# Kernel optimization log

Hardware: AMD Instinct MI355X
Metric: run time of the kernel (lower is better)

## Reference

```python
import jax, jax.numpy as jnp
import numpy as np

LATENT, HIDDEN, NF, MAXN = 256, 512, 64, 50
B = 128
# ordered node pairs (i, j), i != j, in the original double-loop (row-major) order
_pairs = np.array([(i, j) for i in range(MAXN) for j in range(MAXN) if i != j], dtype=np.int32)
II = jnp.asarray(_pairs[:, 0])  # [P]
JJ = jnp.asarray(_pairs[:, 1])  # [P]


def _lin_init(key, out_d, in_d):
    kw, kb = jax.random.split(key)
    s = 1.0 / np.sqrt(in_d)
    W = jax.random.uniform(kw, (out_d, in_d), jnp.float32, -s, s)
    b = jax.random.uniform(kb, (out_d,), jnp.float32, -s, s)
    return W, b


def setup_inputs() -> dict:
    key = jax.random.key(0)
    ks = jax.random.split(key, 7)
    z = jax.random.normal(ks[0], (B, LATENT), jnp.float32)
    # node decoder: latent -> hidden -> hidden -> maxn*nf
    W1, b1 = _lin_init(ks[1], HIDDEN, LATENT)
    W2, b2 = _lin_init(ks[2], HIDDEN, HIDDEN)
    W3, b3 = _lin_init(ks[3], MAXN * NF, HIDDEN)
    # edge decoder: latent + 2*nf -> hidden -> hidden//2 -> 1
    E1, c1 = _lin_init(ks[4], HIDDEN, LATENT + 2 * NF)
    E2, c2 = _lin_init(ks[5], HIDDEN // 2, HIDDEN)
    E3, c3 = _lin_init(ks[6], 1, HIDDEN // 2)
    return {"z": z, "W1": W1, "b1": b1, "W2": W2, "b2": b2, "W3": W3, "b3": b3,
            "E1": E1, "c1": c1, "E2": E2, "c2": c2, "E3": E3, "c3": c3}


def reference(z, W1, b1, W2, b2, W3, b3, E1, c1, E2, c2, E3, c3):
    # ---- node decoder ----
    h = jax.nn.relu(z @ W1.T + b1)
    h = jax.nn.relu(h @ W2.T + b2)
    node_feat = (h @ W3.T + b3).reshape(B, MAXN, NF)  # raw logits used for edges
    node_probs = jax.nn.sigmoid(node_feat)
    # ---- edge decoder: batched over all P = MAXN*(MAXN-1) ordered pairs ----
    ni = node_feat[:, II, :]  # [B, P, NF]
    nj = node_feat[:, JJ, :]  # [B, P, NF]
    P = II.shape[0]
    zb = jnp.broadcast_to(z[:, None, :], (B, P, LATENT))
    edge_in = jnp.concatenate([zb, ni, nj], axis=-1)  # [B, P, LATENT+2*NF]
    e = jax.nn.relu(jnp.einsum("bpf,hf->bph", edge_in, E1) + c1)
    e = jax.nn.relu(jnp.einsum("bph,gh->bpg", e, E2) + c2)
    edge_probs = jax.nn.sigmoid(jnp.einsum("bpg,og->bpo", e, E3) + c3)[..., 0]  # [B, P]
    return node_probs, edge_probs
```

## Files before the change

### kernel.cpp

```cpp
#include <hip/hip_runtime.h>
#include <hip/hip_bf16.h>
#include <math.h>

#define LATENT 256
#define HIDDEN 512
#define NFD    64
#define MAXN   50
#define BATCH  128
#define NPAIR  2450
#define PTILE  64
#define NTILES 39

typedef __attribute__((ext_vector_type(8))) _Float16 f16x8;
typedef __attribute__((ext_vector_type(4))) float f32x4;
typedef __attribute__((ext_vector_type(4))) unsigned int u32x4;

__device__ __forceinline__ float sigmoidf_(float x) {
    return 1.0f / (1.0f + expf(-x));
}
__device__ __forceinline__ f16x8 build_e1(f16x8 ui, f16x8 uj) {
    f16x8 s = ui + uj;
    return __builtin_elementwise_max(s, (f16x8)(_Float16)0);
}
__device__ __forceinline__ void gll16(const void* g, void* l) {
    __builtin_amdgcn_global_load_lds(
        (const __attribute__((address_space(1))) void*)g,
        (__attribute__((address_space(3))) void*)l, 16, 0, 0);
}
__device__ __forceinline__ u32x4 pack8(float4 a, float4 b) {
    f16x8 h;
    h[0] = (_Float16)a.x; h[1] = (_Float16)a.y;
    h[2] = (_Float16)a.z; h[3] = (_Float16)a.w;
    h[4] = (_Float16)b.x; h[5] = (_Float16)b.y;
    h[6] = (_Float16)b.z; h[7] = (_Float16)b.w;
    return __builtin_bit_cast(u32x4, h);
}

__global__ __launch_bounds__(256) void prologue_a(
    const float* __restrict__ z,
    const float* __restrict__ W1, const float* __restrict__ b1,
    const float* __restrict__ E1, const float* __restrict__ c1,
    const float* __restrict__ E2, const float* __restrict__ W2,
    const float* __restrict__ W3,
    unsigned short* __restrict__ E2t,
    unsigned short* __restrict__ W2h,
    unsigned short* __restrict__ W3h,
    unsigned short* __restrict__ E1ih,
    unsigned short* __restrict__ E1jh,
    unsigned short* __restrict__ h1h, float* __restrict__ Abc)
{
    const int tid = threadIdx.x;

    if (blockIdx.x >= 32) {
        int slot = (blockIdx.x - 32) * 4 + blockIdx.y;
        int e = (slot * 256 + tid) * 8;
        const float* src;
        unsigned short* dst;
        if (e < 262144) { src = W2 + e; dst = W2h + e; }
        else if (e < 1900544) { int l = e - 262144; src = W3 + l; dst = W3h + l; }
        else if (e < 1933312) {
            int l = e - 1900544; int row = l >> 6, col = l & 63;
            src = E1 + row * 384 + 256 + col; dst = E1ih + l;
        } else {
            int l = e - 1933312; int row = l >> 6, col = l & 63;
            src = E1 + row * 384 + 320 + col; dst = E1jh + l;
        }
        float4 a = *(const float4*)src;
        float4 b = *(const float4*)(src + 4);
        *(u32x4*)dst = pack8(a, b);
        return;
    }

    if (blockIdx.x >= 16) {
        int idx = ((blockIdx.x - 16) * 4 + blockIdx.y) * 256 + tid;
        int g  = idx & 255;
        int kc = idx >> 8;
        float4 a = *(const float4*)&E2[(size_t)g * 512 + kc * 8];
        float4 b = *(const float4*)&E2[(size_t)g * 512 + kc * 8 + 4];
        *(u32x4*)(E2t + (size_t)idx * 8) = pack8(a, b);
        return;
    }

    __shared__ __align__(16) float As[16][34];
    __shared__ __align__(16) float Bs[16][68];

    const int m0 = blockIdx.y * 32;
    const int n0 = blockIdx.x * 64;
    const bool isE = n0 >= 512;
    const float* Bp = isE ? E1 + (size_t)(n0 - 512) * 384 : W1 + (size_t)n0 * 256;
    const int ldb = isE ? 384 : 256;

    const int sra = tid >> 3;
    const int kca = (tid & 7) * 2;
    const int srb = tid >> 2;
    const int kcb = (tid & 3) * 4;
    const int tx = tid & 15;
    const int ty = tid >> 4;

    float acc[2][4] = {};

    for (int k0 = 0; k0 < 256; k0 += 16) {
        float2 a2 = *(const float2*)&z[(size_t)(m0 + sra) * 256 + k0 + kca];
        As[kca][sra] = a2.x; As[kca + 1][sra] = a2.y;
        float4 b4 = *(const float4*)&Bp[(size_t)srb * ldb + k0 + kcb];
        Bs[kcb + 0][srb] = b4.x; Bs[kcb + 1][srb] = b4.y;
        Bs[kcb + 2][srb] = b4.z; Bs[kcb + 3][srb] = b4.w;
        __syncthreads();
        #pragma unroll
        for (int k = 0; k < 16; ++k) {
            float av[2], bv[4];
            av[0] = As[k][ty * 2]; av[1] = As[k][ty * 2 + 1];
            *(float4*)bv = *(const float4*)&Bs[k][tx * 4];
            #pragma unroll
            for (int r = 0; r < 2; ++r)
                #pragma unroll
                for (int c = 0; c < 4; ++c)
                    acc[r][c] = fmaf(av[r], bv[c], acc[r][c]);
        }
        __syncthreads();
    }

    #pragma unroll
    for (int r = 0; r < 2; ++r) {
        int gm = m0 + ty * 2 + r;
        #pragma unroll
        for (int c = 0; c < 4; ++c) {
            int gn = n0 + tx * 4 + c;
            if (isE) {
                int gl = gn - 512;
                Abc[(size_t)gm * 512 + gl] = acc[r][c] + c1[gl];
            } else {
                float v = fmaxf(acc[r][c] + b1[gn], 0.f);
                h1h[(size_t)gm * 512 + gn] =
                    __builtin_bit_cast(unsigned short, (_Float16)v);
            }
        }
    }
}

__global__ __launch_bounds__(256) void h2_gemm(
    const unsigned short* __restrict__ h1h,
    const unsigned short* __restrict__ W2h,
    const float* __restrict__ b2,
    unsigned short* __restrict__ h2h)
{
    __shared__ unsigned short Ah[3][2048];
    __shared__ unsigned short Bh[3][2048];

    const int tid = threadIdx.x;
    const int lane = tid & 63;
    const int w = tid >> 6;
    const int ln = lane & 15;
    const int hi = lane >> 4;
    const int m0 = blockIdx.y * 64;
    const int n0 = blockIdx.x * 64;

    const int srow = lane >> 2;
    const int scol = (lane & 3) * 8;
    const unsigned short* gA = h1h + (size_t)(m0 + 16 * w + srow) * 512 + scol;
    const unsigned short* gB = W2h + (size_t)(n0 + 16 * w + srow) * 512 + scol;
    unsigned short* lA = (unsigned short*)&Ah[0][0] + 512 * w;
    unsigned short* lB = (unsigned short*)&Bh[0][0] + 512 * w;

    f32x4 acc[4] = {};

    gll16(gA,      lA);          gll16(gB,      lB);
    gll16(gA + 32, lA + 2048);   gll16(gB + 32, lB + 2048);
    asm volatile("s_waitcnt vmcnt(2) lgkmcnt(0)\n\ts_barrier" ::: "memory");

    #pragma unroll
    for (int ks = 0; ks < 16; ++ks) {
        if (ks < 14) {
            const int bn = (ks + 2) % 3;
            gll16(gA + (ks + 2) * 32, lA + bn * 2048);
            gll16(gB + (ks + 2) * 32, lB + bn * 2048);
        }
        const int bb = ks % 3;
        f16x8 af = *(const f16x8*)&Ah[bb][(16 * w + ln) * 32 + hi * 8];
        f16x8 bf[4];
        #pragma unroll
        for (int ni = 0; ni < 4; ++ni)
            bf[ni] = *(const f16x8*)&Bh[bb][(16 * ni + ln) * 32 + hi * 8];
        #pragma unroll
        for (int ni = 0; ni < 4; ++ni)
            acc[ni] = __builtin_amdgcn_mfma_f32_16x16x32_f16(af, bf[ni], acc[ni], 0, 0, 0);
        if (ks < 14) {
            asm volatile("s_waitcnt vmcnt(2) lgkmcnt(0)\n\ts_barrier" ::: "memory");
        } else if (ks == 14) {
            asm volatile("s_waitcnt vmcnt(0) lgkmcnt(0)\n\ts_barrier" ::: "memory");
        }
    }

    #pragma unroll
    for (int ni = 0; ni < 4; ++ni) {
        int gn = n0 + 16 * ni + ln;
        float bias = b2[gn];
        #pragma unroll
        for (int r = 0; r < 4; ++r) {
            int gm = m0 + 16 * w + 4 * hi + r;
            float v = fmaxf(acc[ni][r] + bias, 0.f);
            h2h[(size_t)gm * 512 + gn] =
                __builtin_bit_cast(unsigned short, (_Float16)v);
        }
    }
}

__global__ __launch_bounds__(256) void nfu_gemm(
    const unsigned short* __restrict__ h2h,
    const unsigned short* __restrict__ W3h,
    const float* __restrict__ b3,
    const unsigned short* __restrict__ E1ih,
    const unsigned short* __restrict__ E1jh,
    const float* __restrict__ Abc,
    float* __restrict__ outN,
    unsigned short* __restrict__ Uih,
    unsigned short* __restrict__ Ujh)
{
    __shared__ unsigned short Ah[3][2048];
    __shared__ unsigned short Bh[3][2048];
    __shared__ __align__(16) unsigned short nft[64][72];

    const int tid = threadIdx.x;
    const int lane = tid & 63;
    const int w = tid >> 6;
    const int ln = lane & 15;
    const int hi = lane >> 4;
    const int node = blockIdx.x;
    const int m0 = blockIdx.y * 64;

    const int srow = lane >> 2;
    const int scol = (lane & 3) * 8;
    const unsigned short* gA = h2h + (size_t)(m0 + 16 * w + srow) * 512 + scol;
    const unsigned short* gB = W3h + (size_t)(node * 64 + 16 * w + srow) * 512 + scol;
    unsigned short* lA = (unsigned short*)&Ah[0][0] + 512 * w;
    unsigned short* lB = (unsigned short*)&Bh[0][0] + 512 * w;

    f32x4 acc[4] = {};

    gll16(gA,      lA);          gll16(gB,      lB);
    gll16(gA + 32, lA + 2048);   gll16(gB + 32, lB + 2048);
    asm volatile("s_waitcnt vmcnt(2) lgkmcnt(0)\n\ts_barrier" ::: "memory");

    #pragma unroll
    for (int ks = 0; ks < 16; ++ks) {
        if (ks < 14) {
            const int bn = (ks + 2) % 3;
            gll16(gA + (ks + 2) * 32, lA + bn * 2048);
            gll16(gB + (ks + 2) * 32, lB + bn * 2048);
        }
        const int bb = ks % 3;
        f16x8 af = *(const f16x8*)&Ah[bb][(16 * w + ln) * 32 + hi * 8];
        f16x8 bf[4];
        #pragma unroll
        for (int ni = 0; ni < 4; ++ni)
            bf[ni] = *(const f16x8*)&Bh[bb][(16 * ni + ln) * 32 + hi * 8];
        #pragma unroll
        for (int ni = 0; ni < 4; ++ni)
            acc[ni] = __builtin_amdgcn_mfma_f32_16x16x32_f16(af, bf[ni], acc[ni], 0, 0, 0);
        if (ks < 14) {
            asm volatile("s_waitcnt vmcnt(2) lgkmcnt(0)\n\ts_barrier" ::: "memory");
        } else if (ks == 14) {
            asm volatile("s_waitcnt vmcnt(0) lgkmcnt(0)\n\ts_barrier" ::: "memory");
        }
    }

    #pragma unroll
    for (int ni = 0; ni < 4; ++ni) {
        int gnl = 16 * ni + ln;
        int gng = node * 64 + gnl;
        float bias = b3[gng];
        #pragma unroll
        for (int r = 0; r < 4; ++r) {
            int bl = 16 * w + 4 * hi + r;
            float v = acc[ni][r] + bias;
            outN[(size_t)(m0 + bl) * 3200 + gng] = sigmoidf_(v);
            nft[bl][gnl] = __builtin_bit_cast(unsigned short, (_Float16)v);
        }
    }
    __syncthreads();

    f16x8 af2[2][4];
    #pragma unroll
    for (int ks2 = 0; ks2 < 2; ++ks2)
        #pragma unroll
        for (int mi = 0; mi < 4; ++mi)
            af2[ks2][mi] = *(const f16x8*)&nft[16 * mi + ln][ks2 * 32 + hi * 8];

    #pragma unroll
    for (int ij = 0; ij < 2; ++ij) {
        const unsigned short* Ep = ij ? E1jh : E1ih;
        unsigned short* Ud = ij ? Ujh : Uih;
        #pragma unroll
        for (int half = 0; half < 2; ++half) {
            f32x4 acc2[4][4] = {};
            #pragma unroll
            for (int ks2 = 0; ks2 < 2; ++ks2) {
                f16x8 bf2[4];
                #pragma unroll
                for (int ni = 0; ni < 4; ++ni)
                    bf2[ni] = *(const f16x8*)(Ep +
                        (size_t)(128 * w + half * 64 + 16 * ni + ln) * 64 +
                        ks2 * 32 + hi * 8);
                #pragma unroll
                for (int ni = 0; ni < 4; ++ni)
                    #pragma unroll
                    for (int mi = 0; mi < 4; ++mi)
                        acc2[mi][ni] = __builtin_amdgcn_mfma_f32_16x16x32_f16(
                            af2[ks2][mi], bf2[ni], acc2[mi][ni], 0, 0, 0);
            }
            #pragma unroll
            for (int mi = 0; mi < 4; ++mi) {
                #pragma unroll
                for (int r = 0; r < 4; ++r) {
                    int batch = m0 + 16 * mi + 4 * hi + r;
                    #pragma unroll
                    for (int ni = 0; ni < 4; ++ni) {
                        int h = 128 * w + half * 64 + 16 * ni + ln;
                        float v = acc2[mi][ni][r];
                        if (ij == 0) v += Abc[(size_t)batch * 512 + h];
                        Ud[((size_t)batch * 50 + node) * 512 + h] =
                            __builtin_bit_cast(unsigned short, (_Float16)v);
                    }
                }
            }
        }
    }
}

__global__ __launch_bounds__(256, 4) void edge_mfma(
    const unsigned short* __restrict__ Ui,
    const unsigned short* __restrict__ Uj,
    const unsigned short* __restrict__ E2t,
    const float* __restrict__ c2,
    const float* __restrict__ E3,
    const float* __restrict__ c3p,
    float* __restrict__ outE)
{
    __shared__ unsigned short As[2][PTILE * 32];
    __shared__ float c2_s[256], e3_s[256];
    __shared__ int   ii_s[PTILE], jj_s[PTILE];
    __shared__ float red[PTILE][5];

    const int gid = blockIdx.x;
    const int nid = (gid & 7) * 624 + (gid >> 3);
    const int b   = nid / NTILES;
    const int p0  = (nid - b * NTILES) * PTILE;

    const int tid = threadIdx.x;
    const int lane = tid & 63;
    const int wid  = tid >> 6;
    const int ln = lane & 15;
    const int hi = lane >> 4;

    c2_s[tid] = c2[tid];
    e3_s[tid] = E3[tid];
    if (tid < PTILE) {
        int p = p0 + tid;
        int i = 0, j = 0;
        if (p < NPAIR) {
            i = p / 49;
            int kk = p - i * 49;
            j = kk + (kk >= i ? 1 : 0);
        }
        ii_s[tid] = i;
        jj_s[tid] = j;
    }
    __syncthreads();

    const unsigned short* UiB = Ui + (size_t)b * MAXN * HIDDEN;
    const unsigned short* UjB = Uj + (size_t)b * MAXN * HIDDEN;

    const int srow = tid >> 2;
    const int sc   = tid & 3;
    const unsigned short* gUi = UiB + (size_t)ii_s[srow] * HIDDEN + sc * 8;
    const unsigned short* gUj = UjB + (size_t)jj_s[srow] * HIDDEN + sc * 8;
    const int swr = srow * 32 + ((sc ^ ((srow >> 1) & 3)) * 8);

    const int q   = hi ^ ((ln >> 1) & 3);
    const int ard = ln * 32 + q * 8;

    const unsigned short* bB = E2t + ((size_t)hi * 256 + 64 * wid + ln) * 8;

    f32x4 acc[4][4] = {};

    {
        f16x8 u0 = *(const f16x8*)gUi;
        f16x8 v0 = *(const f16x8*)gUj;
        *(f16x8*)&As[0][swr] = build_e1(u0, v0);
    }
    f16x8 uiN = *(const f16x8*)(gUi + 32);
    f16x8 ujN = *(const f16x8*)(gUj + 32);
    f16x8 bf[4];
    #pragma unroll
    for (int ni = 0; ni < 4; ++ni)
        bf[ni] = *(const f16x8*)(bB + ni * 128);
    asm volatile("s_waitcnt lgkmcnt(0)\n\ts_barrier" ::: "memory");

    #pragma unroll
    for (int ks = 0; ks < 16; ++ks) {
        if (ks < 15)
            *(f16x8*)&As[(ks + 1) & 1][swr] = build_e1(uiN, ujN);
        if (ks < 14) {
            uiN = *(const f16x8*)(gUi + 32 * (ks + 2));
            ujN = *(const f16x8*)(gUj + 32 * (ks + 2));
        }
        f16x8 af[4];
        #pragma unroll
        for (int mi = 0; mi < 4; ++mi)
            af[mi] = *(const f16x8*)&As[ks & 1][ard + mi * 512];
        __builtin_amdgcn_s_setprio(1);
        #pragma unroll
        for (int ni = 0; ni < 4; ++ni)
            #pragma unroll
            for (int mi = 0; mi < 4; ++mi)
                acc[mi][ni] = __builtin_amdgcn_mfma_f32_16x16x32_f16(
                    af[mi], bf[ni], acc[mi][ni], 0, 0, 0);
        __builtin_amdgcn_s_setprio(0);
        if (ks < 15) {
            #pragma unroll
            for (int ni = 0; ni < 4; ++ni)
                bf[ni] = *(const f16x8*)(bB + (size_t)(ks + 1) * 8192 + ni * 128);
            asm volatile("s_waitcnt lgkmcnt(0)\n\ts_barrier" ::: "memory");
        }
    }

    const float c3v = c3p[0];
    #pragma unroll
    for (int mi = 0; mi < 4; ++mi) {
        #pragma unroll
        for (int r = 0; r < 4; ++r) {
            float part = 0.f;
            #pragma unroll
            for (int ni = 0; ni < 4; ++ni) {
                int g = 64 * wid + 16 * ni + ln;
                float v = fmaxf(acc[mi][ni][r] + c2_s[g], 0.f);
                part = fmaf(v, e3_s[g], part);
            }
            part += __shfl_xor(part, 1);
            part += __shfl_xor(part, 2);
            part += __shfl_xor(part, 4);
            part += __shfl_xor(part, 8);
            if (ln == 0) red[16 * mi + 4 * hi + r][wid] = part;
        }
    }
    __syncthreads();

    if (tid < PTILE) {
        int p = p0 + tid;
        if (p < NPAIR) {
            float s = red[tid][0] + red[tid][1] + red[tid][2] + red[tid][3] + c3v;
            outE[(size_t)b * NPAIR + p] = sigmoidf_(s);
        }
    }
}

extern "C" void kernel_launch(void* const* d_in, const int* in_sizes, int n_in,
                              void* d_out, int out_size, void* d_ws, size_t ws_size,
                              hipStream_t stream)
{
    const float* z  = (const float*)d_in[0];
    const float* W1 = (const float*)d_in[1];
    const float* b1 = (const float*)d_in[2];
    const float* W2 = (const float*)d_in[3];
    const float* b2 = (const float*)d_in[4];
    const float* W3 = (const float*)d_in[5];
    const float* b3 = (const float*)d_in[6];
    const float* E1 = (const float*)d_in[7];
    const float* c1 = (const float*)d_in[8];
    const float* E2 = (const float*)d_in[9];
    const float* c2 = (const float*)d_in[10];
    const float* E3 = (const float*)d_in[11];
    const float* c3 = (const float*)d_in[12];

    float* out = (float*)d_out;
    float* ws  = (float*)d_ws;

    float* Abc = ws;
    unsigned short* h1h  = (unsigned short*)(Abc + 65536);
    unsigned short* h2h  = h1h + 65536;
    unsigned short* W2h  = h2h + 65536;
    unsigned short* W3h  = W2h + 262144;
    unsigned short* E1ih = W3h + 1638400;
    unsigned short* E1jh = E1ih + 32768;
    unsigned short* E2t  = E1jh + 32768;
    unsigned short* Uih  = E2t + 131072;
    unsigned short* Ujh  = Uih + 3276800;

    dim3 blk(256);

    prologue_a<<<dim3(272, 4), blk, 0, stream>>>(
        z, W1, b1, E1, c1, E2, W2, W3, E2t, W2h, W3h, E1ih, E1jh, h1h, Abc);

    h2_gemm<<<dim3(8, 2), blk, 0, stream>>>(h1h, W2h, b2, h2h);

    nfu_gemm<<<dim3(50, 2), blk, 0, stream>>>(
        h2h, W3h, b3, E1ih, E1jh, Abc, out, Uih, Ujh);

    edge_mfma<<<dim3(NTILES * BATCH), blk, 0, stream>>>(
        Uih, Ujh, E2t, c2, E3, c3, out + BATCH * MAXN * NFD);
}
```

Baseline: 127.4 us.

## Fuse h2 GEMM into node-feature kernel with MFMA-friendly pre-transposed weights

Removes the separate h2_gemm launch by having each node-feature block recompute its 64-row slice of the second hidden layer into shared memory before the W3 and E1 projections. W2 and W3 are re-laid out in the prologue into an 8-element k-chunk-major format so B fragments load directly from global memory without LDS staging. The block grows to 512 threads, with eight waves sharing the h2 GEMM and four doing the rest. This cuts a launch and the h2 global round trip, but repeats the W2 GEMM work across the 50 node blocks.

```diff
diff --git a/kernel.cpp b/kernel.cpp
--- a/kernel.cpp
+++ b/kernel.cpp
@@ -22,11 +22,6 @@
     f16x8 s = ui + uj;
     return __builtin_elementwise_max(s, (f16x8)(_Float16)0);
 }
-__device__ __forceinline__ void gll16(const void* g, void* l) {
-    __builtin_amdgcn_global_load_lds(
-        (const __attribute__((address_space(1))) void*)g,
-        (__attribute__((address_space(3))) void*)l, 16, 0, 0);
-}
 __device__ __forceinline__ u32x4 pack8(float4 a, float4 b) {
     f16x8 h;
     h[0] = (_Float16)a.x; h[1] = (_Float16)a.y;
@@ -43,8 +38,8 @@
     const float* __restrict__ E2, const float* __restrict__ W2,
     const float* __restrict__ W3,
     unsigned short* __restrict__ E2t,
-    unsigned short* __restrict__ W2h,
-    unsigned short* __restrict__ W3h,
+    unsigned short* __restrict__ W2t,
+    unsigned short* __restrict__ W3t,
     unsigned short* __restrict__ E1ih,
     unsigned short* __restrict__ E1jh,
     unsigned short* __restrict__ h1h, float* __restrict__ Abc)
@@ -54,19 +49,31 @@
     if (blockIdx.x >= 32) {
         int slot = (blockIdx.x - 32) * 4 + blockIdx.y;
         int e = (slot * 256 + tid) * 8;
-        const float* src;
+        float4 a, b;
         unsigned short* dst;
-        if (e < 262144) { src = W2 + e; dst = W2h + e; }
-        else if (e < 1900544) { int l = e - 262144; src = W3 + l; dst = W3h + l; }
-        else if (e < 1933312) {
+        if (e < 262144) {
+            int row = e >> 9, k = e & 511;
+            a = *(const float4*)&W2[e];
+            b = *(const float4*)&W2[e + 4];
+            dst = W2t + (((k >> 3) * 512 + row) << 3);
+        } else if (e < 1900544) {
+            int l = e - 262144;
+            int grow = l >> 9, k = l & 511;
+            int node = grow >> 6, row = grow & 63;
+            a = *(const float4*)&W3[l];
+            b = *(const float4*)&W3[l + 4];
+            dst = W3t + node * 32768 + (((k >> 3) * 64 + row) << 3);
+        } else if (e < 1933312) {
             int l = e - 1900544; int row = l >> 6, col = l & 63;
-            src = E1 + row * 384 + 256 + col; dst = E1ih + l;
+            a = *(const float4*)&E1[row * 384 + 256 + col];
+            b = *(const float4*)&E1[row * 384 + 260 + col];
+            dst = E1ih + l;
         } else {
             int l = e - 1933312; int row = l >> 6, col = l & 63;
-            src = E1 + row * 384 + 320 + col; dst = E1jh + l;
-        }
-        float4 a = *(const float4*)src;
-        float4 b = *(const float4*)(src + 4);
+            a = *(const float4*)&E1[row * 384 + 320 + col];
+            b = *(const float4*)&E1[row * 384 + 324 + col];
+            dst = E1jh + l;
+        }
         *(u32x4*)dst = pack8(a, b);
         return;
     }
@@ -138,76 +145,11 @@
     }
 }
 
-__global__ __launch_bounds__(256) void h2_gemm(
+__global__ __launch_bounds__(512, 1) void nfu_gemm(
     const unsigned short* __restrict__ h1h,
-    const unsigned short* __restrict__ W2h,
+    const unsigned short* __restrict__ W2t,
     const float* __restrict__ b2,
-    unsigned short* __restrict__ h2h)
-{
-    __shared__ unsigned short Ah[3][2048];
-    __shared__ unsigned short Bh[3][2048];
-
-    const int tid = threadIdx.x;
-    const int lane = tid & 63;
-    const int w = tid >> 6;
-    const int ln = lane & 15;
-    const int hi = lane >> 4;
-    const int m0 = blockIdx.y * 64;
-    const int n0 = blockIdx.x * 64;
-
-    const int srow = lane >> 2;
-    const int scol = (lane & 3) * 8;
-    const unsigned short* gA = h1h + (size_t)(m0 + 16 * w + srow) * 512 + scol;
-    const unsigned short* gB = W2h + (size_t)(n0 + 16 * w + srow) * 512 + scol;
-    unsigned short* lA = (unsigned short*)&Ah[0][0] + 512 * w;
-    unsigned short* lB = (unsigned short*)&Bh[0][0] + 512 * w;
-
-    f32x4 acc[4] = {};
-
-    gll16(gA,      lA);          gll16(gB,      lB);
-    gll16(gA + 32, lA + 2048);   gll16(gB + 32, lB + 2048);
-    asm volatile("s_waitcnt vmcnt(2) lgkmcnt(0)\n\ts_barrier" ::: "memory");
-
-    #pragma unroll
-    for (int ks = 0; ks < 16; ++ks) {
-        if (ks < 14) {
-            const int bn = (ks + 2) % 3;
-            gll16(gA + (ks + 2) * 32, lA + bn * 2048);
-            gll16(gB + (ks + 2) * 32, lB + bn * 2048);
-        }
-        const int bb = ks % 3;
-        f16x8 af = *(const f16x8*)&Ah[bb][(16 * w + ln) * 32 + hi * 8];
-        f16x8 bf[4];
-        #pragma unroll
-        for (int ni = 0; ni < 4; ++ni)
-            bf[ni] = *(const f16x8*)&Bh[bb][(16 * ni + ln) * 32 + hi * 8];
-        #pragma unroll
-        for (int ni = 0; ni < 4; ++ni)
-            acc[ni] = __builtin_amdgcn_mfma_f32_16x16x32_f16(af, bf[ni], acc[ni], 0, 0, 0);
-        if (ks < 14) {
-            asm volatile("s_waitcnt vmcnt(2) lgkmcnt(0)\n\ts_barrier" ::: "memory");
-        } else if (ks == 14) {
-            asm volatile("s_waitcnt vmcnt(0) lgkmcnt(0)\n\ts_barrier" ::: "memory");
-        }
-    }
-
-    #pragma unroll
-    for (int ni = 0; ni < 4; ++ni) {
-        int gn = n0 + 16 * ni + ln;
-        float bias = b2[gn];
-        #pragma unroll
-        for (int r = 0; r < 4; ++r) {
-            int gm = m0 + 16 * w + 4 * hi + r;
-            float v = fmaxf(acc[ni][r] + bias, 0.f);
-            h2h[(size_t)gm * 512 + gn] =
-                __builtin_bit_cast(unsigned short, (_Float16)v);
-        }
-    }
-}
-
-__global__ __launch_bounds__(256) void nfu_gemm(
-    const unsigned short* __restrict__ h2h,
-    const unsigned short* __restrict__ W3h,
+    const unsigned short* __restrict__ W3t,
     const float* __restrict__ b3,
     const unsigned short* __restrict__ E1ih,
     const unsigned short* __restrict__ E1jh,
@@ -216,110 +158,155 @@
     unsigned short* __restrict__ Uih,
     unsigned short* __restrict__ Ujh)
 {
-    __shared__ unsigned short Ah[3][2048];
-    __shared__ unsigned short Bh[3][2048];
+    __shared__ unsigned short As[2][64 * 32];
+    __shared__ __align__(16) unsigned short h2s[64][520];
     __shared__ __align__(16) unsigned short nft[64][72];
 
     const int tid = threadIdx.x;
     const int lane = tid & 63;
-    const int w = tid >> 6;
+    const int w8 = tid >> 6;
+    const int w  = w8 & 3;
     const int ln = lane & 15;
     const int hi = lane >> 4;
     const int node = blockIdx.x;
     const int m0 = blockIdx.y * 64;
 
-    const int srow = lane >> 2;
-    const int scol = (lane & 3) * 8;
-    const unsigned short* gA = h2h + (size_t)(m0 + 16 * w + srow) * 512 + scol;
-    const unsigned short* gB = W3h + (size_t)(node * 64 + 16 * w + srow) * 512 + scol;
-    unsigned short* lA = (unsigned short*)&Ah[0][0] + 512 * w;
-    unsigned short* lB = (unsigned short*)&Bh[0][0] + 512 * w;
-
-    f32x4 acc[4] = {};
-
-    gll16(gA,      lA);          gll16(gB,      lB);
-    gll16(gA + 32, lA + 2048);   gll16(gB + 32, lB + 2048);
-    asm volatile("s_waitcnt vmcnt(2) lgkmcnt(0)\n\ts_barrier" ::: "memory");
+    const int srow = (tid & 255) >> 2;
+    const int sc   = tid & 3;
+    const unsigned short* gA = h1h + (size_t)(m0 + srow) * 512 + sc * 8;
+    const int swr = srow * 32 + ((sc ^ ((srow >> 1) & 3)) * 8);
+    const int q   = hi ^ ((ln >> 1) & 3);
+    const int ard = ln * 32 + q * 8;
+    const unsigned short* bB = W2t + ((size_t)hi * 512 + 64 * w8 + ln) * 8;
+
+    f32x4 acc[4][4] = {};
+    f16x8 hN = {};
+    if (tid < 256) {
+        f16x8 h0 = *(const f16x8*)gA;
+        *(f16x8*)&As[0][swr] = h0;
+        hN = *(const f16x8*)(gA + 32);
+    }
+    f16x8 bf[4];
+    #pragma unroll
+    for (int ni = 0; ni < 4; ++ni)
+        bf[ni] = *(const f16x8*)(bB + ni * 128);
+    asm volatile("s_waitcnt lgkmcnt(0)\n\ts_barrier" ::: "memory");
 
     #pragma unroll
     for (int ks = 0; ks < 16; ++ks) {
-        if (ks < 14) {
-            const int bn = (ks + 2) % 3;
-            gll16(gA + (ks + 2) * 32, lA + bn * 2048);
-            gll16(gB + (ks + 2) * 32, lB + bn * 2048);
-        }
-        const int bb = ks % 3;
-        f16x8 af = *(const f16x8*)&Ah[bb][(16 * w + ln) * 32 + hi * 8];
-        f16x8 bf[4];
+        if (tid < 256 && ks < 15)
+            *(f16x8*)&As[(ks + 1) & 1][swr] = hN;
+        if (tid < 256 && ks < 14)
+            hN = *(const f16x8*)(gA + 32 * (ks + 2));
+        f16x8 af[4];
+        #pragma unroll
+        for (int mi = 0; mi < 4; ++mi)
+            af[mi] = *(const f16x8*)&As[ks & 1][ard + mi * 512];
+        __builtin_amdgcn_s_setprio(1);
         #pragma unroll
         for (int ni = 0; ni < 4; ++ni)
-            bf[ni] = *(const f16x8*)&Bh[bb][(16 * ni + ln) * 32 + hi * 8];
-        #pragma unroll
-        for (int ni = 0; ni < 4; ++ni)
-            acc[ni] = __builtin_amdgcn_mfma_f32_16x16x32_f16(af, bf[ni], acc[ni], 0, 0, 0);
-        if (ks < 14) {
-            asm volatile("s_waitcnt vmcnt(2) lgkmcnt(0)\n\ts_barrier" ::: "memory");
-        } else if (ks == 14) {
-            asm volatile("s_waitcnt vmcnt(0) lgkmcnt(0)\n\ts_barrier" ::: "memory");
+            #pragma unroll
+            for (int mi = 0; mi < 4; ++mi)
+                acc[mi][ni] = __builtin_amdgcn_mfma_f32_16x16x32_f16(
+                    af[mi], bf[ni], acc[mi][ni], 0, 0, 0);
+        __builtin_amdgcn_s_setprio(0);
+        if (ks < 15) {
+            #pragma unroll
+            for (int ni = 0; ni < 4; ++ni)
+                bf[ni] = *(const f16x8*)(bB + (size_t)(ks + 1) * 16384 + ni * 128);
+            asm volatile("s_waitcnt lgkmcnt(0)\n\ts_barrier" ::: "memory");
         }
     }
 
     #pragma unroll
     for (int ni = 0; ni < 4; ++ni) {
-        int gnl = 16 * ni + ln;
-        int gng = node * 64 + gnl;
-        float bias = b3[gng];
-        #pragma unroll
-        for (int r = 0; r < 4; ++r) {
-            int bl = 16 * w + 4 * hi + r;
-            float v = acc[ni][r] + bias;
-            outN[(size_t)(m0 + bl) * 3200 + gng] = sigmoidf_(v);
-            nft[bl][gnl] = __builtin_bit_cast(unsigned short, (_Float16)v);
-        }
+        int col = 64 * w8 + 16 * ni + ln;
+        float bias = b2[col];
+        #pragma unroll
+        for (int mi = 0; mi < 4; ++mi)
+            #pragma unroll
+            for (int r = 0; r < 4; ++r) {
+                float v = fmaxf(acc[mi][ni][r] + bias, 0.f);
+                h2s[16 * mi + 4 * hi + r][col] =
+                    __builtin_bit_cast(unsigned short, (_Float16)v);
+            }
     }
     __syncthreads();
 
-    f16x8 af2[2][4];
-    #pragma unroll
-    for (int ks2 = 0; ks2 < 2; ++ks2)
-        #pragma unroll
-        for (int mi = 0; mi < 4; ++mi)
-            af2[ks2][mi] = *(const f16x8*)&nft[16 * mi + ln][ks2 * 32 + hi * 8];
-
-    #pragma unroll
-    for (int ij = 0; ij < 2; ++ij) {
-        const unsigned short* Ep = ij ? E1jh : E1ih;
-        unsigned short* Ud = ij ? Ujh : Uih;
-        #pragma unroll
-        for (int half = 0; half < 2; ++half) {
-            f32x4 acc2[4][4] = {};
-            #pragma unroll
-            for (int ks2 = 0; ks2 < 2; ++ks2) {
-                f16x8 bf2[4];
+    if (w8 < 4) {
+        const unsigned short* bW3 = W3t + (size_t)node * 32768 + hi * 512 + ln * 8;
+        f32x4 accB[4] = {};
+        #pragma unroll
+        for (int ks = 0; ks < 16; ++ks) {
+            f16x8 af = *(const f16x8*)&h2s[16 * w + ln][ks * 32 + hi * 8];
+            f16x8 bfB[4];
+            #pragma unroll
+            for (int ni = 0; ni < 4; ++ni)
+                bfB[ni] = *(const f16x8*)(bW3 + ks * 2048 + ni * 128);
+            #pragma unroll
+            for (int ni = 0; ni < 4; ++ni)
+                accB[ni] = __builtin_amdgcn_mfma_f32_16x16x32_f16(
+                    af, bfB[ni], accB[ni], 0, 0, 0);
+        }
+        #pragma unroll
+        for (int ni = 0; ni < 4; ++ni) {
+            int gnl = 16 * ni + ln;
+            int gng = node * 64 + gnl;
+            float bias = b3[gng];
+            #pragma unroll
+            for (int r = 0; r < 4; ++r) {
+                int bl = 16 * w + 4 * hi + r;
+                float v = accB[ni][r] + bias;
+                outN[(size_t)(m0 + bl) * 3200 + gng] = sigmoidf_(v);
+                nft[bl][gnl] = __builtin_bit_cast(unsigned short, (_Float16)v);
+            }
+        }
+    }
+    __syncthreads();
+
+    if (w8 < 4) {
+        f16x8 af2[2][4];
+        #pragma unroll
+        for (int ks2 = 0; ks2 < 2; ++ks2)
+            #pragma unroll
+            for (int mi = 0; mi < 4; ++mi)
+                af2[ks2][mi] = *(const f16x8*)&nft[16 * mi + ln][ks2 * 32 + hi * 8];
+
+        #pragma unroll
+        for (int ij = 0; ij < 2; ++ij) {
+            const unsigned short* Ep = ij ? E1jh : E1ih;
+            unsigned short* Ud = ij ? Ujh : Uih;
+            #pragma unroll
+            for (int half = 0; half < 2; ++half) {
+                f32x4 acc2[4][4] = {};
                 #pragma unroll
-                for (int ni = 0; ni < 4; ++ni)
-                    bf2[ni] = *(const f16x8*)(Ep +
-                        (size_t)(128 * w + half * 64 + 16 * ni + ln) * 64 +
-                        ks2 * 32 + hi * 8);
+                for (int ks2 = 0; ks2 < 2; ++ks2) {
+                    f16x8 bf2[4];
+                    #pragma unroll
+                    for (int ni = 0; ni < 4; ++ni)
+                        bf2[ni] = *(const f16x8*)(Ep +
+                            (size_t)(128 * w + half * 64 + 16 * ni + ln) * 64 +
+                            ks2 * 32 + hi * 8);
+                    #pragma unroll
+                    for (int ni = 0; ni < 4; ++ni)
+                        #pragma unroll
+                        for (int mi = 0; mi < 4; ++mi)
+                            acc2[mi][ni] = __builtin_amdgcn_mfma_f32_16x16x32_f16(
+                                af2[ks2][mi], bf2[ni], acc2[mi][ni], 0, 0, 0);
+                }
                 #pragma unroll
-                for (int ni = 0; ni < 4; ++ni)
+                for (int mi = 0; mi < 4; ++mi) {
                     #pragma unroll
-                    for (int mi = 0; mi < 4; ++mi)
-                        acc2[mi][ni] = __builtin_amdgcn_mfma_f32_16x16x32_f16(
-                            af2[ks2][mi], bf2[ni], acc2[mi][ni], 0, 0, 0);
-            }
-            #pragma unroll
-            for (int mi = 0; mi < 4; ++mi) {
-                #pragma unroll
-                for (int r = 0; r < 4; ++r) {
-                    int batch = m0 + 16 * mi + 4 * hi + r;
-                    #pragma unroll
-                    for (int ni = 0; ni < 4; ++ni) {
-                        int h = 128 * w + half * 64 + 16 * ni + ln;
-                        float v = acc2[mi][ni][r];
-                        if (ij == 0) v += Abc[(size_t)batch * 512 + h];
-                        Ud[((size_t)batch * 50 + node) * 512 + h] =
-                            __builtin_bit_cast(unsigned short, (_Float16)v);
+                    for (int r = 0; r < 4; ++r) {
+                        int batch = m0 + 16 * mi + 4 * hi + r;
+                        #pragma unroll
+                        for (int ni = 0; ni < 4; ++ni) {
+                            int h = 128 * w + half * 64 + 16 * ni + ln;
+                            float v = acc2[mi][ni][r];
+                            if (ij == 0) v += Abc[(size_t)batch * 512 + h];
+                            Ud[((size_t)batch * 50 + node) * 512 + h] =
+                                __builtin_bit_cast(unsigned short, (_Float16)v);
+                        }
                     }
                 }
             }
@@ -477,10 +464,9 @@
 
     float* Abc = ws;
     unsigned short* h1h  = (unsigned short*)(Abc + 65536);
-    unsigned short* h2h  = h1h + 65536;
-    unsigned short* W2h  = h2h + 65536;
-    unsigned short* W3h  = W2h + 262144;
-    unsigned short* E1ih = W3h + 1638400;
+    unsigned short* W2t  = h1h + 65536;
+    unsigned short* W3t  = W2t + 262144;
+    unsigned short* E1ih = W3t + 1638400;
     unsigned short* E1jh = E1ih + 32768;
     unsigned short* E2t  = E1jh + 32768;
     unsigned short* Uih  = E2t + 131072;
@@ -489,12 +475,10 @@
     dim3 blk(256);
 
     prologue_a<<<dim3(272, 4), blk, 0, stream>>>(
-        z, W1, b1, E1, c1, E2, W2, W3, E2t, W2h, W3h, E1ih, E1jh, h1h, Abc);
-
-    h2_gemm<<<dim3(8, 2), blk, 0, stream>>>(h1h, W2h, b2, h2h);
-
-    nfu_gemm<<<dim3(50, 2), blk, 0, stream>>>(
-        h2h, W3h, b3, E1ih, E1jh, Abc, out, Uih, Ujh);
+        z, W1, b1, E1, c1, E2, W2, W3, E2t, W2t, W3t, E1ih, E1jh, h1h, Abc);
+
+    nfu_gemm<<<dim3(50, 2), dim3(512), 0, stream>>>(
+        h1h, W2t, b2, W3t, b3, E1ih, E1jh, Abc, out, Uih, Ujh);
 
     edge_mfma<<<dim3(NTILES * BATCH), blk, 0, stream>>>(
         Uih, Ujh, E2t, c2, E3, c3, out + BATCH * MAXN * NFD);
```

New measurement: 124.7 us, median of 2. 1.02x faster.
